# Performance work log

Measured on AMD Instinct MI355X. Metric: run time of the kernel, lower is better.

The kernel has to match this reference:

```python
import jax, jax.numpy as jnp
import numpy as np

# Sizes: B graphs of N nodes each, K nearest neighbours, D=feat_dim=nhid, C=pos_dim
B, N, K, D, C = 4, 1024, 128, 32, 2
L = 3                     # number of EGNN conv layers
E_IN = 2 * D + 1          # edge MLP input: feats_i | feats_j | rel_dist (edge_dim=0, fourier=0)
E_H = 2 * E_IN            # edge MLP hidden


def _lin(key, fan_in, fan_out):
    kw, kb = jax.random.split(key)
    w = jax.random.normal(kw, (fan_in, fan_out), jnp.float32) / np.sqrt(fan_in)
    b = jax.random.normal(kb, (fan_out,), jnp.float32) * 0.01
    return w, b


def _stack(key, fan_in, fan_out):
    ws, bs = zip(*[_lin(k, fan_in, fan_out) for k in jax.random.split(key, L)])
    return jnp.stack(ws), jnp.stack(bs)


def setup_inputs() -> dict:
    key = jax.random.key(0)
    ks = jax.random.split(key, 10)
    feat_ = jax.random.normal(ks[0], (B * N, D), jnp.float32)
    coor_ = jax.random.normal(ks[1], (B * N, C), jnp.float32)
    batch = jnp.full((B,), N, dtype=jnp.int32)   # per-graph node counts (equal-size graphs)
    embed_w, embed_b = _lin(ks[2], D, D)         # embed: Linear(feat_dim, nhid)
    e1_w, e1_b = _stack(ks[3], E_IN, E_H)        # edge MLP
    e2_w, e2_b = _stack(ks[4], E_H, D)           # -> m_dim = nhid
    gate_w, gate_b = _stack(ks[5], D, 1)         # soft_edges gate
    c1_w, c1_b = _stack(ks[6], D, 4 * D)         # coors MLP
    c2_w, c2_b = _stack(ks[7], 4 * D, 1)
    n1_w, n1_b = _stack(ks[8], 2 * D, 2 * D)     # node MLP
    n2_w, n2_b = _stack(ks[9], 2 * D, D)
    coors_scale = jnp.full((L, 1), 1e-2, jnp.float32)  # CoorsNorm scale (init 1e-2)
    return dict(feat_=feat_, coor_=coor_, batch=batch, embed_w=embed_w, embed_b=embed_b,
                e1_w=e1_w, e1_b=e1_b, e2_w=e2_w, e2_b=e2_b, gate_w=gate_w, gate_b=gate_b,
                c1_w=c1_w, c1_b=c1_b, c2_w=c2_w, c2_b=c2_b, n1_w=n1_w, n1_b=n1_b,
                n2_w=n2_w, n2_b=n2_b, coors_scale=coors_scale)


def _lrelu(x):
    return jax.nn.leaky_relu(x, 0.1)


def _gather(x, idx):
    # x: [B, n, d], idx: [B, n, k] -> [B, n, k, d]
    return jax.vmap(lambda xb, ib: xb[ib])(x, idx)


def _egnn_layer(feats, coors, p):
    (e1_w, e1_b, e2_w, e2_b, gate_w, gate_b, c1_w, c1_b, c2_w, c2_b,
     n1_w, n1_b, n2_w, n2_b, scale) = p
    # pairwise squared distances; k smallest (self included, valid_radius=inf)
    diff = coors[:, :, None, :] - coors[:, None, :, :]      # [B,n,n,C]
    dist = jnp.sum(diff * diff, axis=-1)                    # [B,n,n]
    neg_d, idx = jax.lax.top_k(-dist, K)                    # k nearest
    rel_dist = -neg_d[..., None]                            # [B,n,K,1]
    rel_coors = coors[:, :, None, :] - _gather(coors, idx)  # [B,n,K,C]
    feats_j = _gather(feats, idx)                           # [B,n,K,D]
    feats_i = jnp.broadcast_to(feats[:, :, None, :], feats_j.shape)
    edge_in = jnp.concatenate([feats_i, feats_j, rel_dist], axis=-1)  # [B,n,K,E_IN]
    # edge MLP: Lin -> act -> Lin -> act ; soft edge gate
    m = _lrelu(_lrelu(edge_in @ e1_w + e1_b) @ e2_w + e2_b)            # [B,n,K,D]
    m = m * jax.nn.sigmoid(m @ gate_w + gate_b)
    # coordinate update: coors_mlp -> scalar weights; CoorsNorm on rel coords
    cw = (_lrelu(m @ c1_w + c1_b) @ c2_w + c2_b)[..., 0]               # [B,n,K]
    norm = jnp.maximum(jnp.linalg.norm(rel_coors, axis=-1, keepdims=True), 1e-8)
    rel_n = rel_coors / norm * scale
    coors_out = jnp.einsum('bik,bikc->bic', cw, rel_n) + coors
    # feature update: sum-pool messages, node MLP with residual
    m_i = jnp.sum(m, axis=2)                                           # [B,n,D]
    node_in = jnp.concatenate([feats, m_i], axis=-1)
    feats_out = _lrelu(node_in @ n1_w + n1_b) @ n2_w + n2_b + feats
    return feats_out, coors_out


def reference(feat_, coor_, batch, embed_w, embed_b, e1_w, e1_b, e2_w, e2_b,
              gate_w, gate_b, c1_w, c1_b, c2_w, c2_b, n1_w, n1_b, n2_w, n2_b,
              coors_scale):
    # embed MLP (dropout is identity at p=0 / eval), then batch equal-size graphs
    feats = _lrelu(feat_ @ embed_w + embed_b).reshape(B, N, D)
    coors = coor_.reshape(B, N, C)
    for l in range(L):
        p = (e1_w[l], e1_b[l], e2_w[l], e2_b[l], gate_w[l], gate_b[l],
             c1_w[l], c1_b[l], c2_w[l], c2_b[l], n1_w[l], n1_b[l],
             n2_w[l], n2_b[l], coors_scale[l])
        feats, coors = _egnn_layer(feats, coors, p)
    return feats.reshape(B * N, D)
```

## Files before the change

kernel.cpp:

```cpp
#include <hip/hip_runtime.h>
#include <hip/hip_bf16.h>
#include <math.h>

#define BB 4
#define NN 1024
#define KK 128
#define DD 32
#define LL 3
#define EH 130
#define EHP 132

typedef float f32x4 __attribute__((ext_vector_type(4)));
typedef short s16x8 __attribute__((ext_vector_type(8)));

__device__ __forceinline__ float lrelu(float x) { return fmaxf(x, 0.1f * x); }

__device__ __forceinline__ unsigned pk2(float a, float b) {
    __hip_bfloat162 h = __float22bfloat162_rn(float2{a, b});
    return *(unsigned*)&h;
}
__device__ __forceinline__ unsigned short bf16_hu(float v) {
    return (unsigned short)((__float_as_uint(v) + 0x8000u) >> 16);
}
__device__ __forceinline__ unsigned short bf16_rne(float v) {
    unsigned u = __float_as_uint(v);
    return (unsigned short)((u + 0x7fffu + ((u >> 16) & 1u)) >> 16);
}

__global__ __launch_bounds__(256) void prep_kernel(
    const float* __restrict__ feat, const float* __restrict__ ew, const float* __restrict__ eb,
    float* __restrict__ out,
    const float* __restrict__ e2w, const float* __restrict__ c1w,
    unsigned short* __restrict__ e2f, unsigned short* __restrict__ c1f) {
    if (blockIdx.x < 512) {
        int t = blockIdx.x * 256 + threadIdx.x;
        if (t >= BB * NN * DD) return;
        int n = t >> 5, o = t & 31;
        const float* f = feat + n * DD;
        float a = eb[o];
#pragma unroll
        for (int k = 0; k < DD; k++) a = fmaf(f[k], ew[k * DD + o], a);
        out[t] = lrelu(a);
    } else {
        int t = (blockIdx.x - 512) * 256 + threadIdx.x;
        if (t < LL * 4 * 2 * 512) {
            int jj = t & 7, lane = (t >> 3) & 63, nt = (t >> 9) & 1, c = (t >> 10) & 3, l = t >> 12;
            int k = 32 * c + (lane >> 4) * 8 + jj;
            int n = nt * 16 + (lane & 15);
            e2f[t] = bf16_rne(e2w[(size_t)l * EH * DD + k * DD + n]);
        } else {
            int u = t - LL * 4 * 2 * 512;
            if (u < LL * 8 * 512) {
                int jj = u & 7, lane = (u >> 3) & 63, nt = (u >> 9) & 7, l = u >> 12;
                int k = (lane >> 4) * 8 + jj;
                int n = nt * 16 + (lane & 15);
                c1f[u] = bf16_rne(c1w[(size_t)l * DD * 128 + k * 128 + n]);
            }
        }
    }
}

__global__ __launch_bounds__(256) void knnpre_kernel(
    const float* __restrict__ coors, int* __restrict__ nbr,
    const float* __restrict__ feats, const float* __restrict__ e1w, const float* __restrict__ e1b,
    float* __restrict__ HI, float* __restrict__ HJ) {
    const int KNNB = BB * NN / 4;
    if (blockIdx.x >= KNNB) {
        int t = (int)(blockIdx.x - KNNB) * 256 + threadIdx.x;
        if (t >= BB * NN * EHP) return;
        int n = t / EHP, o = t % EHP;
        if (o >= EH) { HI[t] = 0.f; HJ[t] = 0.f; return; }
        const float* f = feats + n * DD;
        float a = e1b[o], c = 0.f;
#pragma unroll
        for (int k = 0; k < DD; k++) a = fmaf(f[k], e1w[k * EH + o], a);
#pragma unroll
        for (int k = 0; k < DD; k++) c = fmaf(f[k], e1w[(DD + k) * EH + o], c);
        HI[t] = a;
        HJ[t] = c;
        return;
    }
    const int node = (int)blockIdx.x * 4 + (threadIdx.x >> 6);
    const int b = node >> 10, i = node & (NN - 1);
    const int lane = threadIdx.x & 63;

    const float2* cb = (const float2*)(coors + (size_t)b * NN * 2);
    const float2 ci = cb[i];
    unsigned k[16];
#pragma unroll
    for (int s = 0; s < 16; s++) {
        float2 cj = cb[lane + 64 * s];
        float dx = ci.x - cj.x, dy = ci.y - cj.y;
        float d = __fadd_rn(__fmul_rn(dx, dx), __fmul_rn(dy, dy));
        k[s] = __float_as_uint(d);
    }

    unsigned P = 0;
    for (int bpos = 30; bpos >= 0; bpos--) {
        const unsigned X = P | (1u << bpos);
        unsigned c = 0;
#pragma unroll
        for (int s = 0; s < 16; s++)
            c += (unsigned)__popcll(__ballot(k[s] < X));
        if (c < (unsigned)KK) P = X;
    }
    const unsigned dstar = P;

    const unsigned long long below = (1ull << lane) - 1ull;
    int* nb = nbr + (size_t)node * KK;
    unsigned run = 0;
#pragma unroll
    for (int s = 0; s < 16; s++) {
        unsigned long long m = __ballot(k[s] < dstar);
        if (k[s] < dstar) nb[run + (unsigned)__popcll(m & below)] = lane + 64 * s;
        run += (unsigned)__popcll(m);
    }

    const int need = KK - (int)run;
    unsigned tie = 0;
    for (int s = 0; s < 16 && (int)tie < need; s++) {
        unsigned long long m = __ballot(k[s] == dstar);
        if (k[s] == dstar) {
            unsigned r = tie + (unsigned)__popcll(m & below);
            if ((int)r < need) nb[run + r] = lane + 64 * s;
        }
        tie += (unsigned)__popcll(m);
    }
}

__global__ __launch_bounds__(128) void layer_kernel(
    const float* __restrict__ feats_in, const float* __restrict__ coors_in,
    const int*   __restrict__ nbr,
    const float* __restrict__ HI, const float* __restrict__ HJ,
    const float* __restrict__ w65,
    const float* __restrict__ e2w,
    const float* __restrict__ e2b,
    const unsigned short* __restrict__ e2f,
    const unsigned short* __restrict__ c1f,
    const float* __restrict__ gw, const float* __restrict__ gb,
    const float* __restrict__ c1b, const float* __restrict__ c2w, const float* __restrict__ c2b,
    const float* __restrict__ n1w, const float* __restrict__ n1b,
    const float* __restrict__ n2w, const float* __restrict__ n2b,
    const float* __restrict__ scale,
    float* __restrict__ feats_out, float* __restrict__ coors_out) {
    const int node = blockIdx.x;
    const int b = node >> 10;
    const int t = threadIdx.x;
    const int lane = t & 63, wid = t >> 6;
    const int ln = lane & 15, q = lane >> 4;
    const int rowbase = wid * 64;

    __shared__ __align__(16) float shi[EHP];
    __shared__ __align__(16) float sw65[EHP];
    __shared__ __align__(16) unsigned short smA[2 * 64 * 32];
    __shared__ float sx0[128], sx1[128], su[128], sv[128];
    __shared__ float sgw[DD], se2b[DD], sfi[DD];
    __shared__ float sc1b[128], sc2w[128];
    __shared__ float redm[2][DD], redc[2][2];
    __shared__ float sni[2 * DD], shd[2 * DD];

    for (int u = t; u < EHP; u += 128) {
        shi[u] = HI[(size_t)node * EHP + u];
        sw65[u] = (u < EH) ? w65[u] : 0.f;
    }
    if (t < DD) { sfi[t] = feats_in[node * DD + t]; sgw[t] = gw[t]; se2b[t] = e2b[t]; }
    sc1b[t] = c1b[t];
    sc2w[t] = c2w[t];
    __syncthreads();

    const float cix = coors_in[node * 2], ciy = coors_in[node * 2 + 1];
    const int j = nbr[(size_t)node * KK + t];
    const float2 cj = *(const float2*)(coors_in + ((size_t)(b * NN) + j) * 2);
    const float dx = cix - cj.x, dy = ciy - cj.y;
    const float rd = __fadd_rn(__fmul_rn(dx, dx), __fmul_rn(dy, dy));
    const float nrm = fmaxf(sqrtf(rd), 1e-8f);
    const float s = scale[0] / nrm;
    su[t] = dx * s;
    sv[t] = dy * s;

    {
        const float2 hjt = *(const float2*)(HJ + ((size_t)(b * NN) + j) * EHP + 128);
        sx0[t] = lrelu(shi[128] + hjt.x + rd * sw65[128]);
        sx1[t] = lrelu(shi[129] + hjt.y + rd * sw65[129]);
    }

    const float* hjb[4];
    float rdR[4];
#pragma unroll
    for (int mt = 0; mt < 4; mt++) {
        int jR = __shfl(j, mt * 16 + ln, 64);
        rdR[mt] = __shfl(rd, mt * 16 + ln, 64);
        hjb[mt] = HJ + ((size_t)(b * NN) + jR) * EHP;
    }

    const float4* shi4 = (const float4*)shi;
    const float4* sw4  = (const float4*)sw65;

    const f32x4 zz = {0.f, 0.f, 0.f, 0.f};
    f32x4 accA[4][2];
#pragma unroll
    for (int mt = 0; mt < 4; mt++) { accA[mt][0] = zz; accA[mt][1] = zz; }

    float4 ha[4], hbv[4];
#pragma unroll
    for (int mt = 0; mt < 4; mt++) {
        const float4* hjp = (const float4*)(hjb[mt] + q * 8);
        ha[mt] = hjp[0];
        hbv[mt] = hjp[1];
    }

#pragma unroll 1
    for (int c = 0; c < 4; c++) {
        s16x8 b0 = *(const s16x8*)(e2f + ((c * 2 + 0) * 64 + lane) * 8);
        s16x8 b1 = *(const s16x8*)(e2f + ((c * 2 + 1) * 64 + lane) * 8);
        float4 nha[4], nhb[4];
        if (c < 3) {
#pragma unroll
            for (int mt = 0; mt < 4; mt++) {
                const float4* hjp = (const float4*)(hjb[mt] + (c + 1) * 32 + q * 8);
                nha[mt] = hjp[0];
                nhb[mt] = hjp[1];
            }
        }
        const int kb = c * 8 + q * 2;
        const float4 hi0 = shi4[kb], hi1 = shi4[kb + 1];
        const float4 wv0 = sw4[kb],  wv1 = sw4[kb + 1];
#pragma unroll
        for (int mt = 0; mt < 4; mt++) {
            const float r = rdR[mt];
            union { s16x8 v; unsigned u[4]; } A;
            A.u[0] = pk2(lrelu(hi0.x + ha[mt].x + r * wv0.x), lrelu(hi0.y + ha[mt].y + r * wv0.y));
            A.u[1] = pk2(lrelu(hi0.z + ha[mt].z + r * wv0.z), lrelu(hi0.w + ha[mt].w + r * wv0.w));
            A.u[2] = pk2(lrelu(hi1.x + hbv[mt].x + r * wv1.x), lrelu(hi1.y + hbv[mt].y + r * wv1.y));
            A.u[3] = pk2(lrelu(hi1.z + hbv[mt].z + r * wv1.z), lrelu(hi1.w + hbv[mt].w + r * wv1.w));
            accA[mt][0] = __builtin_amdgcn_mfma_f32_16x16x32_bf16(A.v, b0, accA[mt][0], 0, 0, 0);
            accA[mt][1] = __builtin_amdgcn_mfma_f32_16x16x32_bf16(A.v, b1, accA[mt][1], 0, 0, 0);
        }
#pragma unroll
        for (int mt = 0; mt < 4; mt++) { ha[mt] = nha[mt]; hbv[mt] = nhb[mt]; }
    }

#pragma unroll
    for (int nt = 0; nt < 2; nt++) {
        const int col = nt * 16 + ln;
        const float w128 = e2w[128 * DD + col];
        const float w129 = e2w[129 * DD + col];
        const float bv = se2b[col];
#pragma unroll
        for (int mt = 0; mt < 4; mt++)
#pragma unroll
            for (int r = 0; r < 4; r++) {
                const int row = rowbase + mt * 16 + q * 4 + r;
                accA[mt][nt][r] = lrelu(accA[mt][nt][r] + bv + sx0[row] * w128 + sx1[row] * w129);
            }
    }

    const float gbv = gb[0];
#pragma unroll
    for (int mt = 0; mt < 4; mt++) {
        float p[4];
#pragma unroll
        for (int r = 0; r < 4; r++)
            p[r] = accA[mt][0][r] * sgw[ln] + accA[mt][1][r] * sgw[16 + ln];
#pragma unroll
        for (int off = 1; off <= 8; off <<= 1)
#pragma unroll
            for (int r = 0; r < 4; r++) p[r] += __shfl_xor(p[r], off);
#pragma unroll
        for (int r = 0; r < 4; r++) {
            const float g = 1.f / (1.f + __expf(-(p[r] + gbv)));
            accA[mt][0][r] *= g;
            accA[mt][1][r] *= g;
        }
    }

    float mi0 = 0.f, mi1 = 0.f;
#pragma unroll
    for (int mt = 0; mt < 4; mt++)
#pragma unroll
        for (int r = 0; r < 4; r++) { mi0 += accA[mt][0][r]; mi1 += accA[mt][1][r]; }
    mi0 += __shfl_xor(mi0, 16); mi0 += __shfl_xor(mi0, 32);
    mi1 += __shfl_xor(mi1, 16); mi1 += __shfl_xor(mi1, 32);
    if (lane < 16) { redm[wid][lane] = mi0; redm[wid][16 + lane] = mi1; }

    unsigned short* smw = smA + wid * (64 * 32);
#pragma unroll
    for (int mt = 0; mt < 4; mt++)
#pragma unroll
        for (int nt = 0; nt < 2; nt++)
#pragma unroll
            for (int r = 0; r < 4; r++) {
                const int prow = (r << 4) | (4 * mt + q);
                smw[prow * 32 + nt * 16 + ln] = bf16_hu(accA[mt][nt][r]);
            }

    s16x8 a4[4];
#pragma unroll
    for (int mt = 0; mt < 4; mt++) {
        const int prow = ((ln & 3) << 4) | (4 * mt + (ln >> 2));
        a4[mt] = *(const s16x8*)(smw + prow * 32 + q * 8);
    }

    float cacc[4][4];
#pragma unroll
    for (int mt = 0; mt < 4; mt++)
#pragma unroll
        for (int r = 0; r < 4; r++) cacc[mt][r] = 0.f;

#pragma unroll 1
    for (int g = 0; g < 4; g++) {
        s16x8 bc0 = *(const s16x8*)(c1f + ((2 * g + 0) * 64 + lane) * 8);
        s16x8 bc1 = *(const s16x8*)(c1f + ((2 * g + 1) * 64 + lane) * 8);
        f32x4 c20[4], c21[4];
#pragma unroll
        for (int mt = 0; mt < 4; mt++) {
            c20[mt] = __builtin_amdgcn_mfma_f32_16x16x32_bf16(a4[mt], bc0, zz, 0, 0, 0);
            c21[mt] = __builtin_amdgcn_mfma_f32_16x16x32_bf16(a4[mt], bc1, zz, 0, 0, 0);
        }
#pragma unroll
        for (int h = 0; h < 2; h++) {
            const int col = (2 * g + h) * 16 + ln;
            const float c1bv = sc1b[col], c2wv = sc2w[col];
#pragma unroll
            for (int mt = 0; mt < 4; mt++)
#pragma unroll
                for (int r = 0; r < 4; r++) {
                    const float v = (h ? c21[mt][r] : c20[mt][r]) + c1bv;
                    cacc[mt][r] = fmaf(lrelu(v), c2wv, cacc[mt][r]);
                }
        }
    }
#pragma unroll
    for (int off = 1; off <= 8; off <<= 1)
#pragma unroll
        for (int mt = 0; mt < 4; mt++)
#pragma unroll
            for (int r = 0; r < 4; r++) cacc[mt][r] += __shfl_xor(cacc[mt][r], off);

    const float c2bv = c2b[0];
    float vxp = 0.f, vyp = 0.f;
    if (ln == 0) {
#pragma unroll
        for (int mt = 0; mt < 4; mt++)
#pragma unroll
            for (int r = 0; r < 4; r++) {
                const int row = rowbase + mt * 16 + q * 4 + r;
                const float cw = cacc[mt][r] + c2bv;
                vxp = fmaf(cw, su[row], vxp);
                vyp = fmaf(cw, sv[row], vyp);
            }
    }
    vxp += __shfl_xor(vxp, 16); vxp += __shfl_xor(vxp, 32);
    vyp += __shfl_xor(vyp, 16); vyp += __shfl_xor(vyp, 32);
    if (lane == 0) { redc[wid][0] = vxp; redc[wid][1] = vyp; }

    __syncthreads();
    if (t < DD) {
        sni[t] = sfi[t];
        sni[DD + t] = redm[0][t] + redm[1][t];
    }
    __syncthreads();
    if (t < 2 * DD) {
        float a = n1b[t];
#pragma unroll
        for (int k = 0; k < 2 * DD; k++) a = fmaf(sni[k], n1w[k * 2 * DD + t], a);
        shd[t] = lrelu(a);
    }
    __syncthreads();
    if (t < DD) {
        float a = n2b[t];
#pragma unroll
        for (int o = 0; o < 2 * DD; o++) a = fmaf(shd[o], n2w[o * DD + t], a);
        feats_out[node * DD + t] = a + sfi[t];
    }
    if (t == 0) {
        coors_out[node * 2] = cix + redc[0][0] + redc[1][0];
        coors_out[node * 2 + 1] = ciy + redc[0][1] + redc[1][1];
    }
}

extern "C" void kernel_launch(void* const* d_in, const int* in_sizes, int n_in,
                              void* d_out, int out_size, void* d_ws, size_t ws_size,
                              hipStream_t stream) {
    const float* feat_   = (const float*)d_in[0];
    const float* coor_   = (const float*)d_in[1];
    const float* embed_w = (const float*)d_in[3];
    const float* embed_b = (const float*)d_in[4];
    const float* e1_w    = (const float*)d_in[5];
    const float* e1_b    = (const float*)d_in[6];
    const float* e2_w    = (const float*)d_in[7];
    const float* e2_b    = (const float*)d_in[8];
    const float* gate_w  = (const float*)d_in[9];
    const float* gate_b  = (const float*)d_in[10];
    const float* c1_w    = (const float*)d_in[11];
    const float* c1_b    = (const float*)d_in[12];
    const float* c2_w    = (const float*)d_in[13];
    const float* c2_b    = (const float*)d_in[14];
    const float* n1_w    = (const float*)d_in[15];
    const float* n1_b    = (const float*)d_in[16];
    const float* n2_w    = (const float*)d_in[17];
    const float* n2_b    = (const float*)d_in[18];
    const float* cscale  = (const float*)d_in[19];

    float* ws = (float*)d_ws;
    float* feats_a = ws;               ws += BB * NN * DD;
    float* feats_b = ws;               ws += BB * NN * DD;
    float* coors_a = ws;               ws += BB * NN * 2;
    float* coors_b = ws;               ws += BB * NN * 2;
    float* HI      = ws;               ws += BB * NN * EHP;
    float* HJ      = ws;               ws += BB * NN * EHP;
    unsigned short* e2f = (unsigned short*)ws;
    unsigned short* c1f = e2f + LL * 4096;
    ws += (2 * LL * 4096) / 2;
    int* nbr = (int*)ws;

    prep_kernel<<<512 + 96, 256, 0, stream>>>(feat_, embed_w, embed_b, feats_a,
                                              e2_w, c1_w, e2f, c1f);

    const int KNNB = BB * NN / 4;
    const int PREB = (BB * NN * EHP + 255) / 256;
    const float* fin = feats_a;
    const float* cin = coor_;
    float* fouts[LL] = {feats_b, feats_a, (float*)d_out};
    float* couts[LL] = {coors_a, coors_b, coors_a};

    for (int l = 0; l < LL; l++) {
        knnpre_kernel<<<KNNB + PREB, 256, 0, stream>>>(
            cin, nbr, fin, e1_w + (size_t)l * 65 * EH, e1_b + (size_t)l * EH, HI, HJ);
        layer_kernel<<<BB * NN, 128, 0, stream>>>(
            fin, cin, nbr, HI, HJ,
            e1_w + ((size_t)l * 65 + 64) * EH,
            e2_w + (size_t)l * EH * DD,
            e2_b + (size_t)l * DD,
            e2f + (size_t)l * 4096,
            c1f + (size_t)l * 4096,
            gate_w + (size_t)l * DD,
            gate_b + l,
            c1_b + (size_t)l * 128,
            c2_w + (size_t)l * 128,
            c2_b + l,
            n1_w + (size_t)l * 64 * 64,
            n1_b + (size_t)l * 64,
            n2_w + (size_t)l * 64 * 32,
            n2_b + (size_t)l * DD,
            cscale + l,
            fouts[l], couts[l]);
        fin = fouts[l];
        cin = couts[l];
    }
}
```

Measured before the change: 328.8 us.

## Fuse kNN selection and next-layer edge projections into the layer kernel

```diff
diff --git a/kernel.cpp b/kernel.cpp
--- a/kernel.cpp
+++ b/kernel.cpp
@@ -31,16 +31,35 @@
     const float* __restrict__ feat, const float* __restrict__ ew, const float* __restrict__ eb,
     float* __restrict__ out,
     const float* __restrict__ e2w, const float* __restrict__ c1w,
-    unsigned short* __restrict__ e2f, unsigned short* __restrict__ c1f) {
+    unsigned short* __restrict__ e2f, unsigned short* __restrict__ c1f,
+    const float* __restrict__ e1w0, const float* __restrict__ e1b0,
+    float* __restrict__ HI, float* __restrict__ HJ) {
     if (blockIdx.x < 512) {
-        int t = blockIdx.x * 256 + threadIdx.x;
-        if (t >= BB * NN * DD) return;
-        int n = t >> 5, o = t & 31;
+        const int tid = threadIdx.x;
+        const int t = blockIdx.x * 256 + tid;
+        const int n = t >> 5, o = t & 31;
+        __shared__ float sfe[256];
         const float* f = feat + n * DD;
         float a = eb[o];
 #pragma unroll
         for (int k = 0; k < DD; k++) a = fmaf(f[k], ew[k * DD + o], a);
-        out[t] = lrelu(a);
+        a = lrelu(a);
+        out[t] = a;
+        sfe[tid] = a;
+        __syncthreads();
+        for (int idx = tid; idx < 8 * EHP; idx += 256) {
+            const int nl = idx / EHP, o2 = idx % EHP;
+            const size_t off = (size_t)(blockIdx.x * 8 + nl) * EHP + o2;
+            if (o2 >= EH) { HI[off] = 0.f; HJ[off] = 0.f; continue; }
+            const float* fl = sfe + nl * DD;
+            float aa = e1b0[o2], cc = 0.f;
+#pragma unroll
+            for (int k = 0; k < DD; k++) aa = fmaf(fl[k], e1w0[k * EH + o2], aa);
+#pragma unroll
+            for (int k = 0; k < DD; k++) cc = fmaf(fl[k], e1w0[(DD + k) * EH + o2], cc);
+            HI[off] = aa;
+            HJ[off] = cc;
+        }
     } else {
         int t = (blockIdx.x - 512) * 256 + threadIdx.x;
         if (t < LL * 4 * 2 * 512) {
@@ -60,78 +79,12 @@
     }
 }
 
-__global__ __launch_bounds__(256) void knnpre_kernel(
-    const float* __restrict__ coors, int* __restrict__ nbr,
-    const float* __restrict__ feats, const float* __restrict__ e1w, const float* __restrict__ e1b,
-    float* __restrict__ HI, float* __restrict__ HJ) {
-    const int KNNB = BB * NN / 4;
-    if (blockIdx.x >= KNNB) {
-        int t = (int)(blockIdx.x - KNNB) * 256 + threadIdx.x;
-        if (t >= BB * NN * EHP) return;
-        int n = t / EHP, o = t % EHP;
-        if (o >= EH) { HI[t] = 0.f; HJ[t] = 0.f; return; }
-        const float* f = feats + n * DD;
-        float a = e1b[o], c = 0.f;
-#pragma unroll
-        for (int k = 0; k < DD; k++) a = fmaf(f[k], e1w[k * EH + o], a);
-#pragma unroll
-        for (int k = 0; k < DD; k++) c = fmaf(f[k], e1w[(DD + k) * EH + o], c);
-        HI[t] = a;
-        HJ[t] = c;
-        return;
-    }
-    const int node = (int)blockIdx.x * 4 + (threadIdx.x >> 6);
-    const int b = node >> 10, i = node & (NN - 1);
-    const int lane = threadIdx.x & 63;
-
-    const float2* cb = (const float2*)(coors + (size_t)b * NN * 2);
-    const float2 ci = cb[i];
-    unsigned k[16];
-#pragma unroll
-    for (int s = 0; s < 16; s++) {
-        float2 cj = cb[lane + 64 * s];
-        float dx = ci.x - cj.x, dy = ci.y - cj.y;
-        float d = __fadd_rn(__fmul_rn(dx, dx), __fmul_rn(dy, dy));
-        k[s] = __float_as_uint(d);
-    }
-
-    unsigned P = 0;
-    for (int bpos = 30; bpos >= 0; bpos--) {
-        const unsigned X = P | (1u << bpos);
-        unsigned c = 0;
-#pragma unroll
-        for (int s = 0; s < 16; s++)
-            c += (unsigned)__popcll(__ballot(k[s] < X));
-        if (c < (unsigned)KK) P = X;
-    }
-    const unsigned dstar = P;
-
-    const unsigned long long below = (1ull << lane) - 1ull;
-    int* nb = nbr + (size_t)node * KK;
-    unsigned run = 0;
-#pragma unroll
-    for (int s = 0; s < 16; s++) {
-        unsigned long long m = __ballot(k[s] < dstar);
-        if (k[s] < dstar) nb[run + (unsigned)__popcll(m & below)] = lane + 64 * s;
-        run += (unsigned)__popcll(m);
-    }
-
-    const int need = KK - (int)run;
-    unsigned tie = 0;
-    for (int s = 0; s < 16 && (int)tie < need; s++) {
-        unsigned long long m = __ballot(k[s] == dstar);
-        if (k[s] == dstar) {
-            unsigned r = tie + (unsigned)__popcll(m & below);
-            if ((int)r < need) nb[run + r] = lane + 64 * s;
-        }
-        tie += (unsigned)__popcll(m);
-    }
-}
-
 __global__ __launch_bounds__(128) void layer_kernel(
     const float* __restrict__ feats_in, const float* __restrict__ coors_in,
-    const int*   __restrict__ nbr,
     const float* __restrict__ HI, const float* __restrict__ HJ,
+    float* __restrict__ HIo, float* __restrict__ HJo,
+    const float* __restrict__ e1n, const float* __restrict__ e1bn,
+    const int donext,
     const float* __restrict__ w65,
     const float* __restrict__ e2w,
     const float* __restrict__ e2b,
@@ -144,33 +97,84 @@
     const float* __restrict__ scale,
     float* __restrict__ feats_out, float* __restrict__ coors_out) {
     const int node = blockIdx.x;
-    const int b = node >> 10;
+    const int b = node >> 10, i = node & (NN - 1);
     const int t = threadIdx.x;
     const int lane = t & 63, wid = t >> 6;
     const int ln = lane & 15, q = lane >> 4;
     const int rowbase = wid * 64;
 
+    __shared__ float2 scoor[NN];
+    __shared__ int snbr[KK];
     __shared__ __align__(16) float shi[EHP];
     __shared__ __align__(16) float sw65[EHP];
     __shared__ __align__(16) unsigned short smA[2 * 64 * 32];
     __shared__ float sx0[128], sx1[128], su[128], sv[128];
-    __shared__ float sgw[DD], se2b[DD], sfi[DD];
+    __shared__ float sgw[DD], se2b[DD], sfi[DD], sfo[DD];
     __shared__ float sc1b[128], sc2w[128];
     __shared__ float redm[2][DD], redc[2][2];
     __shared__ float sni[2 * DD], shd[2 * DD];
 
-    for (int u = t; u < EHP; u += 128) {
-        shi[u] = HI[(size_t)node * EHP + u];
-        sw65[u] = (u < EH) ? w65[u] : 0.f;
-    }
-    if (t < DD) { sfi[t] = feats_in[node * DD + t]; sgw[t] = gw[t]; se2b[t] = e2b[t]; }
-    sc1b[t] = c1b[t];
-    sc2w[t] = c2w[t];
+    if (wid == 0) {
+        const float2* cbp = (const float2*)(coors_in + (size_t)b * NN * 2);
+        const float2 ci = cbp[i];
+        unsigned k[16];
+#pragma unroll
+        for (int s = 0; s < 16; s++) {
+            float2 cj = cbp[lane + 64 * s];
+            scoor[lane + 64 * s] = cj;
+            float dx = ci.x - cj.x, dy = ci.y - cj.y;
+            float d = __fadd_rn(__fmul_rn(dx, dx), __fmul_rn(dy, dy));
+            k[s] = __float_as_uint(d);
+        }
+        unsigned P = 0;
+        for (int bpos = 30; bpos >= 0; bpos--) {
+            const unsigned X = P | (1u << bpos);
+            unsigned c = 0;
+#pragma unroll
+            for (int s = 0; s < 16; s++)
+                c += (unsigned)__popcll(__ballot(k[s] < X));
+            if (c < (unsigned)KK) P = X;
+        }
+        const unsigned dstar = P;
+        const unsigned long long below = (1ull << lane) - 1ull;
+        unsigned run = 0;
+#pragma unroll
+        for (int s = 0; s < 16; s++) {
+            unsigned long long m = __ballot(k[s] < dstar);
+            if (k[s] < dstar) snbr[run + (unsigned)__popcll(m & below)] = lane + 64 * s;
+            run += (unsigned)__popcll(m);
+        }
+        const int need = KK - (int)run;
+        unsigned tie = 0;
+        for (int s = 0; s < 16 && (int)tie < need; s++) {
+            unsigned long long m = __ballot(k[s] == dstar);
+            if (k[s] == dstar) {
+                unsigned r = tie + (unsigned)__popcll(m & below);
+                if ((int)r < need) snbr[run + r] = lane + 64 * s;
+            }
+            tie += (unsigned)__popcll(m);
+        }
+    } else {
+        for (int u = lane; u < EHP; u += 64) {
+            shi[u] = HI[(size_t)node * EHP + u];
+            sw65[u] = (u < EH) ? w65[u] : 0.f;
+        }
+        if (lane < DD) {
+            sfi[lane] = feats_in[node * DD + lane];
+            sgw[lane] = gw[lane];
+            se2b[lane] = e2b[lane];
+        }
+        sc1b[lane] = c1b[lane];
+        sc1b[lane + 64] = c1b[lane + 64];
+        sc2w[lane] = c2w[lane];
+        sc2w[lane + 64] = c2w[lane + 64];
+    }
     __syncthreads();
 
-    const float cix = coors_in[node * 2], ciy = coors_in[node * 2 + 1];
-    const int j = nbr[(size_t)node * KK + t];
-    const float2 cj = *(const float2*)(coors_in + ((size_t)(b * NN) + j) * 2);
+    const float2 cif = scoor[i];
+    const float cix = cif.x, ciy = cif.y;
+    const int j = snbr[t];
+    const float2 cj = scoor[j];
     const float dx = cix - cj.x, dy = ciy - cj.y;
     const float rd = __fadd_rn(__fmul_rn(dx, dx), __fmul_rn(dy, dy));
     const float nrm = fmaxf(sqrtf(rd), 1e-8f);
@@ -371,11 +375,28 @@
         float a = n2b[t];
 #pragma unroll
         for (int o = 0; o < 2 * DD; o++) a = fmaf(shd[o], n2w[o * DD + t], a);
-        feats_out[node * DD + t] = a + sfi[t];
+        const float fo = a + sfi[t];
+        feats_out[node * DD + t] = fo;
+        sfo[t] = fo;
     }
     if (t == 0) {
         coors_out[node * 2] = cix + redc[0][0] + redc[1][0];
         coors_out[node * 2 + 1] = ciy + redc[0][1] + redc[1][1];
+    }
+    __syncthreads();
+
+    if (donext) {
+        for (int o = t; o < EHP; o += 128) {
+            const size_t off = (size_t)node * EHP + o;
+            if (o >= EH) { HIo[off] = 0.f; HJo[off] = 0.f; continue; }
+            float aa = e1bn[o], cc = 0.f;
+#pragma unroll
+            for (int k = 0; k < DD; k++) aa = fmaf(sfo[k], e1n[k * EH + o], aa);
+#pragma unroll
+            for (int k = 0; k < DD; k++) cc = fmaf(sfo[k], e1n[(DD + k) * EH + o], cc);
+            HIo[off] = aa;
+            HJo[off] = cc;
+        }
     }
 }
 
@@ -407,28 +428,32 @@
     float* feats_b = ws;               ws += BB * NN * DD;
     float* coors_a = ws;               ws += BB * NN * 2;
     float* coors_b = ws;               ws += BB * NN * 2;
-    float* HI      = ws;               ws += BB * NN * EHP;
-    float* HJ      = ws;               ws += BB * NN * EHP;
+    float* HI_a    = ws;               ws += BB * NN * EHP;
+    float* HJ_a    = ws;               ws += BB * NN * EHP;
+    float* HI_b    = ws;               ws += BB * NN * EHP;
+    float* HJ_b    = ws;               ws += BB * NN * EHP;
     unsigned short* e2f = (unsigned short*)ws;
     unsigned short* c1f = e2f + LL * 4096;
-    ws += (2 * LL * 4096) / 2;
-    int* nbr = (int*)ws;
 
     prep_kernel<<<512 + 96, 256, 0, stream>>>(feat_, embed_w, embed_b, feats_a,
-                                              e2_w, c1_w, e2f, c1f);
-
-    const int KNNB = BB * NN / 4;
-    const int PREB = (BB * NN * EHP + 255) / 256;
+                                              e2_w, c1_w, e2f, c1f,
+                                              e1_w, e1_b, HI_a, HJ_a);
+
     const float* fin = feats_a;
     const float* cin = coor_;
     float* fouts[LL] = {feats_b, feats_a, (float*)d_out};
     float* couts[LL] = {coors_a, coors_b, coors_a};
+    float* HIs[2] = {HI_a, HI_b};
+    float* HJs[2] = {HJ_a, HJ_b};
 
     for (int l = 0; l < LL; l++) {
-        knnpre_kernel<<<KNNB + PREB, 256, 0, stream>>>(
-            cin, nbr, fin, e1_w + (size_t)l * 65 * EH, e1_b + (size_t)l * EH, HI, HJ);
+        const int nl = (l + 1 < LL) ? l + 1 : l;
         layer_kernel<<<BB * NN, 128, 0, stream>>>(
-            fin, cin, nbr, HI, HJ,
+            fin, cin,
+            HIs[l & 1], HJs[l & 1],
+            HIs[(l + 1) & 1], HJs[(l + 1) & 1],
+            e1_w + (size_t)nl * 65 * EH, e1_b + (size_t)nl * EH,
+            (l + 1 < LL) ? 1 : 0,
             e1_w + ((size_t)l * 65 + 64) * EH,
             e2_w + (size_t)l * EH * DD,
             e2_b + (size_t)l * DD,
```

Result: slower. 381.3 us (+15.9%).

## Fuse embed, kNN, precompute and all EGNN layers into one cooperative kernel

Applied to the files above, without the earlier changes.

```diff
diff --git a/kernel.cpp b/kernel.cpp
--- a/kernel.cpp
+++ b/kernel.cpp
@@ -1,6 +1,9 @@
 #include <hip/hip_runtime.h>
 #include <hip/hip_bf16.h>
+#include <hip/hip_cooperative_groups.h>
 #include <math.h>
+
+namespace cg = cooperative_groups;
 
 #define BB 4
 #define NN 1024
@@ -9,6 +12,8 @@
 #define LL 3
 #define EH 130
 #define EHP 132
+#define NPB 4
+#define GRID (BB * NN / NPB)
 
 typedef float f32x4 __attribute__((ext_vector_type(4)));
 typedef short s16x8 __attribute__((ext_vector_type(8)));
@@ -25,6 +30,423 @@
 __device__ __forceinline__ unsigned short bf16_rne(float v) {
     unsigned u = __float_as_uint(v);
     return (unsigned short)((u + 0x7fffu + ((u >> 16) & 1u)) >> 16);
+}
+
+__global__ __launch_bounds__(128, 3) void mega_kernel(
+    const float* __restrict__ feat, const float* __restrict__ coor,
+    const float* __restrict__ ew, const float* __restrict__ ebias,
+    const float* __restrict__ e1w, const float* __restrict__ e1b,
+    const float* __restrict__ e2w, const float* __restrict__ e2b,
+    const float* __restrict__ gw, const float* __restrict__ gb,
+    const float* __restrict__ c1w, const float* __restrict__ c1b,
+    const float* __restrict__ c2w, const float* __restrict__ c2b,
+    const float* __restrict__ n1w, const float* __restrict__ n1b,
+    const float* __restrict__ n2w, const float* __restrict__ n2b,
+    const float* __restrict__ cscale,
+    float* __restrict__ fa, float* __restrict__ fb,
+    float* __restrict__ ca, float* __restrict__ cb2,
+    float* __restrict__ HIa, float* __restrict__ HJa,
+    float* __restrict__ HIb, float* __restrict__ HJb,
+    unsigned short* __restrict__ e2f, unsigned short* __restrict__ c1f,
+    float* __restrict__ dout) {
+    const int bid = blockIdx.x;
+    const int t = threadIdx.x;
+    const int lane = t & 63, wid = t >> 6;
+    const int ln = lane & 15, q = lane >> 4;
+    const int rowbase = wid * 64;
+    const int n0 = bid * NPB;
+    const int b = n0 >> 10;
+
+    __shared__ int snbr[2][KK];
+    __shared__ __align__(16) float sw65[EHP];
+    __shared__ __align__(16) float shi[2][EHP];
+    __shared__ __align__(16) unsigned short smA[2 * 64 * 32];
+    __shared__ float sx0[2][128], sx1[2][128], su[2][128], sv[2][128];
+    __shared__ float sgw[DD], se2b[DD];
+    __shared__ float sfi[2][DD], sfo[2][DD];
+    __shared__ float sc1b[128], sc2w[128];
+    __shared__ float redm[2][2][DD], redc[2][2][2];
+    __shared__ float sni[2 * DD], shd[2 * DD];
+
+    {
+        const int nl = t >> 5, o = t & 31;
+        const float* f = feat + (size_t)(n0 + nl) * DD;
+        float a = ebias[o];
+#pragma unroll
+        for (int k = 0; k < DD; k++) a = fmaf(f[k], ew[k * DD + o], a);
+        a = lrelu(a);
+        fa[(size_t)(n0 + nl) * DD + o] = a;
+        sx0[0][t] = a;
+    }
+    __syncthreads();
+    for (int idx = t; idx < NPB * EHP; idx += 128) {
+        const int nl = idx / EHP, o = idx - nl * EHP;
+        const size_t off = (size_t)(n0 + nl) * EHP + o;
+        if (o >= EH) { HIa[off] = 0.f; HJa[off] = 0.f; continue; }
+        const float* fl = &sx0[0][nl * DD];
+        float aa = e1b[o], cc = 0.f;
+#pragma unroll
+        for (int k = 0; k < DD; k++) aa = fmaf(fl[k], e1w[k * EH + o], aa);
+#pragma unroll
+        for (int k = 0; k < DD; k++) cc = fmaf(fl[k], e1w[(DD + k) * EH + o], cc);
+        HIa[off] = aa;
+        HJa[off] = cc;
+    }
+    if (bid < 96) {
+        for (int u = bid * 128 + t; u < 2 * LL * 4096; u += 96 * 128) {
+            if (u < LL * 4096) {
+                int jj = u & 7, la = (u >> 3) & 63, nt = (u >> 9) & 1, c = (u >> 10) & 3, l = u >> 12;
+                int k = 32 * c + (la >> 4) * 8 + jj;
+                int n = nt * 16 + (la & 15);
+                e2f[u] = bf16_rne(e2w[(size_t)l * EH * DD + k * DD + n]);
+            } else {
+                int v = u - LL * 4096;
+                int jj = v & 7, la = (v >> 3) & 63, nt = (v >> 9) & 7, l = v >> 12;
+                int k = (la >> 4) * 8 + jj;
+                int n = nt * 16 + (la & 15);
+                c1f[v] = bf16_rne(c1w[(size_t)l * DD * 128 + k * 128 + n]);
+            }
+        }
+    }
+    cg::this_grid().sync();
+
+    const float* fin = fa;
+    const float* cin = coor;
+    const float* HIc = HIa;
+    const float* HJc = HJa;
+    float* fouts[LL] = {fb, fa, dout};
+    float* couts[LL] = {ca, cb2, ca};
+
+    for (int l = 0; l < LL; l++) {
+        const float* w65  = e1w + ((size_t)l * 65 + 64) * EH;
+        const float* e2wl = e2w + (size_t)l * EH * DD;
+        const float* e2bl = e2b + (size_t)l * DD;
+        const unsigned short* e2fl = e2f + (size_t)l * 4096;
+        const unsigned short* c1fl = c1f + (size_t)l * 4096;
+        const float* gwl  = gw + (size_t)l * DD;
+        const float  gbv  = gb[l];
+        const float* c1bl = c1b + (size_t)l * 128;
+        const float* c2wl = c2w + (size_t)l * 128;
+        const float  c2bv = c2b[l];
+        const float* n1wl = n1w + (size_t)l * 64 * 64;
+        const float* n1bl = n1b + (size_t)l * 64;
+        const float* n2wl = n2w + (size_t)l * 64 * 32;
+        const float* n2bl = n2b + (size_t)l * DD;
+        const float  scl  = cscale[l];
+        float* HIn = (l & 1) ? HIa : HIb;
+        float* HJn = (l & 1) ? HJa : HJb;
+
+        for (int u = t; u < EHP; u += 128) sw65[u] = (u < EH) ? w65[u] : 0.f;
+        if (t < DD) { sgw[t] = gwl[t]; se2b[t] = e2bl[t]; }
+        sc1b[t] = c1bl[t];
+        sc2w[t] = c2wl[t];
+
+        for (int p = 0; p < NPB / 2; p++) {
+            const int nA = n0 + 2 * p;
+
+            {
+                const int myn = nA + wid;
+                const float2* cbp = (const float2*)cin + (size_t)b * NN;
+                const float2 ci = cbp[myn & (NN - 1)];
+                unsigned kk[16];
+#pragma unroll
+                for (int s = 0; s < 16; s++) {
+                    float2 cj = cbp[lane + 64 * s];
+                    float dx = ci.x - cj.x, dy = ci.y - cj.y;
+                    float d = __fadd_rn(__fmul_rn(dx, dx), __fmul_rn(dy, dy));
+                    kk[s] = __float_as_uint(d);
+                }
+                unsigned P = 0;
+                for (int bpos = 30; bpos >= 0; bpos--) {
+                    const unsigned X = P | (1u << bpos);
+                    unsigned c = 0;
+#pragma unroll
+                    for (int s = 0; s < 16; s++)
+                        c += (unsigned)__popcll(__ballot(kk[s] < X));
+                    if (c < (unsigned)KK) P = X;
+                }
+                const unsigned dstar = P;
+                const unsigned long long below = (1ull << lane) - 1ull;
+                unsigned run = 0;
+#pragma unroll
+                for (int s = 0; s < 16; s++) {
+                    unsigned long long m = __ballot(kk[s] < dstar);
+                    if (kk[s] < dstar) snbr[wid][run + (unsigned)__popcll(m & below)] = lane + 64 * s;
+                    run += (unsigned)__popcll(m);
+                }
+                const int need = KK - (int)run;
+                unsigned tie = 0;
+                for (int s = 0; s < 16 && (int)tie < need; s++) {
+                    unsigned long long m = __ballot(kk[s] == dstar);
+                    if (kk[s] == dstar) {
+                        unsigned r = tie + (unsigned)__popcll(m & below);
+                        if ((int)r < need) snbr[wid][run + r] = lane + 64 * s;
+                    }
+                    tie += (unsigned)__popcll(m);
+                }
+            }
+            __syncthreads();
+
+            for (int u = t; u < EHP; u += 128) {
+                shi[0][u] = HIc[(size_t)nA * EHP + u];
+                shi[1][u] = HIc[(size_t)(nA + 1) * EHP + u];
+            }
+            if (t < DD) {
+                sfi[0][t] = fin[(size_t)nA * DD + t];
+                sfi[1][t] = fin[(size_t)(nA + 1) * DD + t];
+            }
+            __syncthreads();
+
+            int j0, j1;
+            float rd0, rd1;
+#pragma unroll
+            for (int nn = 0; nn < 2; nn++) {
+                const int myn = nA + nn;
+                const float2 ci = ((const float2*)cin)[(size_t)b * NN + (myn & (NN - 1))];
+                const int j = snbr[nn][t];
+                const float2 cj = ((const float2*)cin)[(size_t)b * NN + j];
+                const float dx = ci.x - cj.x, dy = ci.y - cj.y;
+                const float rd = __fadd_rn(__fmul_rn(dx, dx), __fmul_rn(dy, dy));
+                const float nrm = fmaxf(sqrtf(rd), 1e-8f);
+                const float s = scl / nrm;
+                su[nn][t] = dx * s;
+                sv[nn][t] = dy * s;
+                const float2 hjt = *(const float2*)(HJc + ((size_t)(b * NN) + j) * EHP + 128);
+                sx0[nn][t] = lrelu(shi[nn][128] + hjt.x + rd * sw65[128]);
+                sx1[nn][t] = lrelu(shi[nn][129] + hjt.y + rd * sw65[129]);
+                if (nn == 0) { j0 = j; rd0 = rd; } else { j1 = j; rd1 = rd; }
+            }
+            __syncthreads();
+
+#pragma unroll 1
+            for (int nn = 0; nn < 2; nn++) {
+                const int myn = nA + nn;
+                const int jme = nn ? j1 : j0;
+                const float rdme = nn ? rd1 : rd0;
+
+                const float* hjb[4];
+                float rdR[4];
+#pragma unroll
+                for (int mt = 0; mt < 4; mt++) {
+                    int jR = __shfl(jme, mt * 16 + ln, 64);
+                    rdR[mt] = __shfl(rdme, mt * 16 + ln, 64);
+                    hjb[mt] = HJc + ((size_t)(b * NN) + jR) * EHP;
+                }
+
+                const float4* shi4 = (const float4*)shi[nn];
+                const float4* sw4  = (const float4*)sw65;
+
+                const f32x4 zz = {0.f, 0.f, 0.f, 0.f};
+                f32x4 accA[4][2];
+#pragma unroll
+                for (int mt = 0; mt < 4; mt++) { accA[mt][0] = zz; accA[mt][1] = zz; }
+
+                float4 ha[4], hbv[4];
+#pragma unroll
+                for (int mt = 0; mt < 4; mt++) {
+                    const float4* hjp = (const float4*)(hjb[mt] + q * 8);
+                    ha[mt] = hjp[0];
+                    hbv[mt] = hjp[1];
+                }
+
+#pragma unroll 1
+                for (int c = 0; c < 4; c++) {
+                    s16x8 b0 = *(const s16x8*)(e2fl + ((c * 2 + 0) * 64 + lane) * 8);
+                    s16x8 b1 = *(const s16x8*)(e2fl + ((c * 2 + 1) * 64 + lane) * 8);
+                    float4 nha[4], nhb[4];
+                    if (c < 3) {
+#pragma unroll
+                        for (int mt = 0; mt < 4; mt++) {
+                            const float4* hjp = (const float4*)(hjb[mt] + (c + 1) * 32 + q * 8);
+                            nha[mt] = hjp[0];
+                            nhb[mt] = hjp[1];
+                        }
+                    }
+                    const int kb = c * 8 + q * 2;
+                    const float4 hi0 = shi4[kb], hi1 = shi4[kb + 1];
+                    const float4 wv0 = sw4[kb],  wv1 = sw4[kb + 1];
+#pragma unroll
+                    for (int mt = 0; mt < 4; mt++) {
+                        const float r = rdR[mt];
+                        union { s16x8 v; unsigned u[4]; } A;
+                        A.u[0] = pk2(lrelu(hi0.x + ha[mt].x + r * wv0.x), lrelu(hi0.y + ha[mt].y + r * wv0.y));
+                        A.u[1] = pk2(lrelu(hi0.z + ha[mt].z + r * wv0.z), lrelu(hi0.w + ha[mt].w + r * wv0.w));
+                        A.u[2] = pk2(lrelu(hi1.x + hbv[mt].x + r * wv1.x), lrelu(hi1.y + hbv[mt].y + r * wv1.y));
+                        A.u[3] = pk2(lrelu(hi1.z + hbv[mt].z + r * wv1.z), lrelu(hi1.w + hbv[mt].w + r * wv1.w));
+                        accA[mt][0] = __builtin_amdgcn_mfma_f32_16x16x32_bf16(A.v, b0, accA[mt][0], 0, 0, 0);
+                        accA[mt][1] = __builtin_amdgcn_mfma_f32_16x16x32_bf16(A.v, b1, accA[mt][1], 0, 0, 0);
+                    }
+#pragma unroll
+                    for (int mt = 0; mt < 4; mt++) { ha[mt] = nha[mt]; hbv[mt] = nhb[mt]; }
+                }
+
+#pragma unroll
+                for (int nt = 0; nt < 2; nt++) {
+                    const int col = nt * 16 + ln;
+                    const float w128 = e2wl[128 * DD + col];
+                    const float w129 = e2wl[129 * DD + col];
+                    const float bv = se2b[col];
+#pragma unroll
+                    for (int mt = 0; mt < 4; mt++)
+#pragma unroll
+                        for (int r = 0; r < 4; r++) {
+                            const int row = rowbase + mt * 16 + q * 4 + r;
+                            accA[mt][nt][r] = lrelu(accA[mt][nt][r] + bv + sx0[nn][row] * w128 + sx1[nn][row] * w129);
+                        }
+                }
+
+#pragma unroll
+                for (int mt = 0; mt < 4; mt++) {
+                    float p2[4];
+#pragma unroll
+                    for (int r = 0; r < 4; r++)
+                        p2[r] = accA[mt][0][r] * sgw[ln] + accA[mt][1][r] * sgw[16 + ln];
+#pragma unroll
+                    for (int off = 1; off <= 8; off <<= 1)
+#pragma unroll
+                        for (int r = 0; r < 4; r++) p2[r] += __shfl_xor(p2[r], off);
+#pragma unroll
+                    for (int r = 0; r < 4; r++) {
+                        const float g = 1.f / (1.f + __expf(-(p2[r] + gbv)));
+                        accA[mt][0][r] *= g;
+                        accA[mt][1][r] *= g;
+                    }
+                }
+
+                float mi0 = 0.f, mi1 = 0.f;
+#pragma unroll
+                for (int mt = 0; mt < 4; mt++)
+#pragma unroll
+                    for (int r = 0; r < 4; r++) { mi0 += accA[mt][0][r]; mi1 += accA[mt][1][r]; }
+                mi0 += __shfl_xor(mi0, 16); mi0 += __shfl_xor(mi0, 32);
+                mi1 += __shfl_xor(mi1, 16); mi1 += __shfl_xor(mi1, 32);
+                if (lane < 16) { redm[nn][wid][lane] = mi0; redm[nn][wid][16 + lane] = mi1; }
+
+                unsigned short* smw = smA + wid * (64 * 32);
+#pragma unroll
+                for (int mt = 0; mt < 4; mt++)
+#pragma unroll
+                    for (int nt = 0; nt < 2; nt++)
+#pragma unroll
+                        for (int r = 0; r < 4; r++) {
+                            const int prow = (r << 4) | (4 * mt + q);
+                            smw[prow * 32 + nt * 16 + ln] = bf16_hu(accA[mt][nt][r]);
+                        }
+
+                s16x8 a4[4];
+#pragma unroll
+                for (int mt = 0; mt < 4; mt++) {
+                    const int prow = ((ln & 3) << 4) | (4 * mt + (ln >> 2));
+                    a4[mt] = *(const s16x8*)(smw + prow * 32 + q * 8);
+                }
+
+                float cacc[4][4];
+#pragma unroll
+                for (int mt = 0; mt < 4; mt++)
+#pragma unroll
+                    for (int r = 0; r < 4; r++) cacc[mt][r] = 0.f;
+
+#pragma unroll 1
+                for (int g = 0; g < 4; g++) {
+                    s16x8 bc0 = *(const s16x8*)(c1fl + ((2 * g + 0) * 64 + lane) * 8);
+                    s16x8 bc1 = *(const s16x8*)(c1fl + ((2 * g + 1) * 64 + lane) * 8);
+                    f32x4 c20[4], c21[4];
+#pragma unroll
+                    for (int mt = 0; mt < 4; mt++) {
+                        c20[mt] = __builtin_amdgcn_mfma_f32_16x16x32_bf16(a4[mt], bc0, zz, 0, 0, 0);
+                        c21[mt] = __builtin_amdgcn_mfma_f32_16x16x32_bf16(a4[mt], bc1, zz, 0, 0, 0);
+                    }
+#pragma unroll
+                    for (int h = 0; h < 2; h++) {
+                        const int col = (2 * g + h) * 16 + ln;
+                        const float c1bv = sc1b[col], c2wv = sc2w[col];
+#pragma unroll
+                        for (int mt = 0; mt < 4; mt++)
+#pragma unroll
+                            for (int r = 0; r < 4; r++) {
+                                const float v = (h ? c21[mt][r] : c20[mt][r]) + c1bv;
+                                cacc[mt][r] = fmaf(lrelu(v), c2wv, cacc[mt][r]);
+                            }
+                    }
+                }
+#pragma unroll
+                for (int off = 1; off <= 8; off <<= 1)
+#pragma unroll
+                    for (int mt = 0; mt < 4; mt++)
+#pragma unroll
+                        for (int r = 0; r < 4; r++) cacc[mt][r] += __shfl_xor(cacc[mt][r], off);
+
+                float vxp = 0.f, vyp = 0.f;
+                if (ln == 0) {
+#pragma unroll
+                    for (int mt = 0; mt < 4; mt++)
+#pragma unroll
+                        for (int r = 0; r < 4; r++) {
+                            const int row = rowbase + mt * 16 + q * 4 + r;
+                            const float cw = cacc[mt][r] + c2bv;
+                            vxp = fmaf(cw, su[nn][row], vxp);
+                            vyp = fmaf(cw, sv[nn][row], vyp);
+                        }
+                }
+                vxp += __shfl_xor(vxp, 16); vxp += __shfl_xor(vxp, 32);
+                vyp += __shfl_xor(vyp, 16); vyp += __shfl_xor(vyp, 32);
+                if (lane == 0) { redc[nn][wid][0] = vxp; redc[nn][wid][1] = vyp; }
+
+                __syncthreads();
+                if (t < DD) {
+                    sni[t] = sfi[nn][t];
+                    sni[DD + t] = redm[nn][0][t] + redm[nn][1][t];
+                }
+                __syncthreads();
+                if (t < 2 * DD) {
+                    float a = n1bl[t];
+#pragma unroll
+                    for (int k = 0; k < 2 * DD; k++) a = fmaf(sni[k], n1wl[k * 2 * DD + t], a);
+                    shd[t] = lrelu(a);
+                }
+                __syncthreads();
+                if (t < DD) {
+                    float a = n2bl[t];
+#pragma unroll
+                    for (int o = 0; o < 2 * DD; o++) a = fmaf(shd[o], n2wl[o * DD + t], a);
+                    const float fo = a + sfi[nn][t];
+                    fouts[l][(size_t)myn * DD + t] = fo;
+                    sfo[nn][t] = fo;
+                }
+                if (t == 0) {
+                    const float2 cif = ((const float2*)cin)[(size_t)b * NN + (myn & (NN - 1))];
+                    couts[l][(size_t)myn * 2] = cif.x + redc[nn][0][0] + redc[nn][1][0];
+                    couts[l][(size_t)myn * 2 + 1] = cif.y + redc[nn][0][1] + redc[nn][1][1];
+                }
+                __syncthreads();
+            }
+
+            if (l + 1 < LL) {
+                const float* e1n  = e1w + (size_t)(l + 1) * 65 * EH;
+                const float* e1bn = e1b + (size_t)(l + 1) * EH;
+                for (int idx = t; idx < 2 * EHP; idx += 128) {
+                    const int nl = idx / EHP, o = idx - nl * EHP;
+                    const size_t off = (size_t)(nA + nl) * EHP + o;
+                    if (o >= EH) { HIn[off] = 0.f; HJn[off] = 0.f; continue; }
+                    const float* fl = sfo[nl];
+                    float aa = e1bn[o], cc = 0.f;
+#pragma unroll
+                    for (int k = 0; k < DD; k++) aa = fmaf(fl[k], e1n[k * EH + o], aa);
+#pragma unroll
+                    for (int k = 0; k < DD; k++) cc = fmaf(fl[k], e1n[(DD + k) * EH + o], cc);
+                    HIn[off] = aa;
+                    HJn[off] = cc;
+                }
+            }
+            __syncthreads();
+        }
+
+        fin = fouts[l];
+        cin = couts[l];
+        HIc = HIn;
+        HJc = HJn;
+        if (l + 1 < LL) cg::this_grid().sync();
+    }
 }
 
 __global__ __launch_bounds__(256) void prep_kernel(
@@ -94,7 +516,6 @@
         float d = __fadd_rn(__fmul_rn(dx, dx), __fmul_rn(dy, dy));
         k[s] = __float_as_uint(d);
     }
-
     unsigned P = 0;
     for (int bpos = 30; bpos >= 0; bpos--) {
         const unsigned X = P | (1u << bpos);
@@ -105,7 +526,6 @@
         if (c < (unsigned)KK) P = X;
     }
     const unsigned dstar = P;
-
     const unsigned long long below = (1ull << lane) - 1ull;
     int* nb = nbr + (size_t)node * KK;
     unsigned run = 0;
@@ -115,7 +535,6 @@
         if (k[s] < dstar) nb[run + (unsigned)__popcll(m & below)] = lane + 64 * s;
         run += (unsigned)__popcll(m);
     }
-
     const int need = KK - (int)run;
     unsigned tie = 0;
     for (int s = 0; s < 16 && (int)tie < need; s++) {
@@ -403,32 +822,48 @@
     const float* cscale  = (const float*)d_in[19];
 
     float* ws = (float*)d_ws;
-    float* feats_a = ws;               ws += BB * NN * DD;
-    float* feats_b = ws;               ws += BB * NN * DD;
-    float* coors_a = ws;               ws += BB * NN * 2;
-    float* coors_b = ws;               ws += BB * NN * 2;
-    float* HI      = ws;               ws += BB * NN * EHP;
-    float* HJ      = ws;               ws += BB * NN * EHP;
+    float* fa   = ws;   ws += BB * NN * DD;
+    float* fb   = ws;   ws += BB * NN * DD;
+    float* ca   = ws;   ws += BB * NN * 2;
+    float* cb2  = ws;   ws += BB * NN * 2;
+    float* HIa  = ws;   ws += BB * NN * EHP;
+    float* HJa  = ws;   ws += BB * NN * EHP;
+    float* HIb  = ws;   ws += BB * NN * EHP;
+    float* HJb  = ws;   ws += BB * NN * EHP;
     unsigned short* e2f = (unsigned short*)ws;
     unsigned short* c1f = e2f + LL * 4096;
-    ws += (2 * LL * 4096) / 2;
-    int* nbr = (int*)ws;
-
-    prep_kernel<<<512 + 96, 256, 0, stream>>>(feat_, embed_w, embed_b, feats_a,
+    int* nbr = (int*)(c1f + LL * 4096);
+    float* doutp = (float*)d_out;
+
+    void* args[] = {
+        (void*)&feat_, (void*)&coor_, (void*)&embed_w, (void*)&embed_b,
+        (void*)&e1_w, (void*)&e1_b, (void*)&e2_w, (void*)&e2_b,
+        (void*)&gate_w, (void*)&gate_b, (void*)&c1_w, (void*)&c1_b,
+        (void*)&c2_w, (void*)&c2_b, (void*)&n1_w, (void*)&n1_b,
+        (void*)&n2_w, (void*)&n2_b, (void*)&cscale,
+        (void*)&fa, (void*)&fb, (void*)&ca, (void*)&cb2,
+        (void*)&HIa, (void*)&HJa, (void*)&HIb, (void*)&HJb,
+        (void*)&e2f, (void*)&c1f, (void*)&doutp};
+
+    hipError_t cerr = hipLaunchCooperativeKernel((const void*)mega_kernel, dim3(GRID),
+                                                 dim3(128), args, 0, stream);
+    if (cerr == hipSuccess) return;
+    (void)hipGetLastError();
+
+    prep_kernel<<<512 + 96, 256, 0, stream>>>(feat_, embed_w, embed_b, fa,
                                               e2_w, c1_w, e2f, c1f);
-
     const int KNNB = BB * NN / 4;
     const int PREB = (BB * NN * EHP + 255) / 256;
-    const float* fin = feats_a;
+    const float* fin = fa;
     const float* cin = coor_;
-    float* fouts[LL] = {feats_b, feats_a, (float*)d_out};
-    float* couts[LL] = {coors_a, coors_b, coors_a};
+    float* fouts[LL] = {fb, fa, (float*)d_out};
+    float* couts[LL] = {ca, cb2, ca};
 
     for (int l = 0; l < LL; l++) {
         knnpre_kernel<<<KNNB + PREB, 256, 0, stream>>>(
-            cin, nbr, fin, e1_w + (size_t)l * 65 * EH, e1_b + (size_t)l * EH, HI, HJ);
+            cin, nbr, fin, e1_w + (size_t)l * 65 * EH, e1_b + (size_t)l * EH, HIa, HJa);
         layer_kernel<<<BB * NN, 128, 0, stream>>>(
-            fin, cin, nbr, HI, HJ,
+            fin, cin, nbr, HIa, HJa,
             e1_w + ((size_t)l * 65 + 64) * EH,
             e2_w + (size_t)l * EH * DD,
             e2_b + (size_t)l * DD,
```

Result: slower. 1.306 ms (+297.2%).
